# Performance work log

Measured on AMD Instinct MI355X. Metric: run time of the kernel, lower is better.

Reference implementation:

```python
import jax, jax.numpy as jnp
import numpy as np

N = 100_000   # nodes
E = 1_600_000 # message-passing edges
EA = 1_000_000 # aux edges for bilinear head
G = 512       # graphs in batch
F_IN = 16     # num_node_features (fixed in source)
H = 32        # hidden_dim (fixed in source)


def setup_inputs() -> dict:
    key = jax.random.key(0)
    ks = jax.random.split(key, 8)
    x = jax.random.normal(ks[0], (N, F_IN), jnp.float32)
    edge_index = jax.random.randint(ks[1], (2, E), 0, N, dtype=jnp.int32)
    edge_index_aux = jax.random.randint(ks[2], (2, EA), 0, N, dtype=jnp.int32)
    batch = jnp.sort(jax.random.randint(ks[3], (N,), 0, G, dtype=jnp.int32))
    W1 = jax.random.normal(ks[4], (F_IN, H), jnp.float32) / np.sqrt(F_IN)
    b1 = jnp.zeros((H,), jnp.float32)
    W2 = jax.random.normal(ks[5], (H, H), jnp.float32) / np.sqrt(H)
    b2 = jnp.zeros((H,), jnp.float32)
    Wr = jax.random.normal(ks[6], (H, 1), jnp.float32) / np.sqrt(H)
    br = jnp.zeros((1,), jnp.float32)
    Wbil = jax.random.normal(ks[7], (1, H, H), jnp.float32) / H
    bbil = jnp.zeros((1,), jnp.float32)
    return dict(x=x, edge_index=edge_index, edge_index_aux=edge_index_aux,
                batch=batch, W1=W1, b1=b1, W2=W2, b2=b2, Wr=Wr, br=br,
                Wbil=Wbil, bbil=bbil)


def gcn_conv(x, W, b, src, dst):
    # PyG GCNConv: x' = D^{-1/2}(A+I)D^{-1/2} (x W) + b, deg includes self-loop
    xw = x @ W                                                   # [N,H]
    deg = jax.ops.segment_sum(jnp.ones((src.shape[0],), x.dtype), dst,
                              num_segments=N) + 1.0              # +1 self-loop
    dinv = jax.lax.rsqrt(deg)                                    # [N]
    coef = dinv[src] * dinv[dst]                                 # [E]
    agg = jax.ops.segment_sum(xw[src] * coef[:, None], dst, num_segments=N)
    agg = agg + xw * (dinv * dinv)[:, None]                      # self-loop msg
    return agg + b


def reference(x, edge_index, edge_index_aux, batch,
              W1, b1, W2, b2, Wr, br, Wbil, bbil):
    src, dst = edge_index[0], edge_index[1]
    h = jax.nn.relu(gcn_conv(x, W1, b1, src, dst))
    h = gcn_conv(h, W2, b2, src, dst)
    # global_mean_pool over graph ids
    cnt = jax.ops.segment_sum(jnp.ones((N,), h.dtype), batch, num_segments=G)
    pooled = jax.ops.segment_sum(h, batch, num_segments=G) / jnp.maximum(cnt, 1.0)[:, None]
    reg_output = pooled @ Wr + br                                # [G,1]
    # Bilinear edge head: out_e = x1_e^T W x2_e + b
    h1 = h[edge_index_aux[0]]                                    # [EA,H]
    h2 = h[edge_index_aux[1]]                                    # [EA,H]
    edge_pred = jnp.einsum('ei,ij,ej->e', h1, Wbil[0], h2)[:, None] + bbil
    return reg_output, edge_pred
```

## Files before the change

kernel.cpp:

```cpp
#include <hip/hip_runtime.h>
#include <hip/hip_bf16.h>
#include <string.h>
#include <stdint.h>

typedef __hip_bfloat16 bf16;

#define FIN 16
#define H   32
#define PADW 64
#define NB  512
#define BINCAP 4096
#define NPBMAX 200
#define PSTRIDE 65
#define CHUNK 8192
#define SCAN_CHUNK 1024
#define MAXSEG 64
#define POOLBLK 256

__device__ __forceinline__ float b2f(bf16 v) { return __bfloat162float(v); }

__device__ __forceinline__ float loadf(const void* p, size_t i, int f32) {
    return f32 ? ((const float*)p)[i] : b2f(((const bf16*)p)[i]);
}
__device__ __forceinline__ void storef(void* p, size_t i, float v, int f32) {
    if (f32) ((float*)p)[i] = v;
    else     ((bf16*)p)[i] = __float2bfloat16(v);
}

__device__ __forceinline__ unsigned pack2(float lo, float hi) {
    bf16 a = __float2bfloat16(lo), b = __float2bfloat16(hi);
    unsigned short ua, ub;
    memcpy(&ua, &a, 2); memcpy(&ub, &b, 2);
    return ((unsigned)ub << 16) | (unsigned)ua;
}
__device__ __forceinline__ float f_lo(unsigned u) {
    union { unsigned i; float f; } v; v.i = u << 16; return v.f;
}
__device__ __forceinline__ float f_hi(unsigned u) {
    union { unsigned i; float f; } v; v.i = u & 0xffff0000u; return v.f;
}

__global__ void k_detect(const void* __restrict__ x, int nelem, int* __restrict__ flag,
                         float* __restrict__ zf, int nzf,
                         int* __restrict__ zi, int nzi) {
    for (int i = threadIdx.x; i < nzf; i += blockDim.x) zf[i] = 0.f;
    if (zi) for (int i = threadIdx.x; i < nzi; i += blockDim.x) zi[i] = 0;
    __shared__ int cntS;
    if (threadIdx.x == 0) cntS = 0;
    __syncthreads();
    int bad = 0;
    const bf16* p = (const bf16*)x;
    for (int i = threadIdx.x; i < nelem; i += blockDim.x) {
        float v = b2f(p[i]);
        float a = fabsf(v);
        if (isnan(v) || a > 1024.f || (v != 0.f && a < 1e-20f)) bad++;
    }
    atomicAdd(&cntS, bad);
    __syncthreads();
    if (threadIdx.x == 0) flag[0] = (cntS > 64) ? 1 : 0;
}

__global__ void __launch_bounds__(1024) k_p1(
        const int* __restrict__ src, const int* __restrict__ dst,
        int* __restrict__ bincur, unsigned* __restrict__ binbuf,
        int E, int npb) {
    __shared__ int hcnt[4][NB];
    __shared__ int hbase[NB];
    __shared__ int scur[NB];
    int tid = threadIdx.x;
    int grp = tid >> 8;
    int e0 = blockIdx.x * CHUNK;
    int nE = E - e0;
    if (nE > CHUNK) nE = CHUNK;
    for (int i = tid; i < 4 * NB; i += blockDim.x) ((int*)hcnt)[i] = 0;
    __syncthreads();
    for (int i = tid; i < nE; i += blockDim.x)
        atomicAdd(&hcnt[grp][dst[e0 + i] / npb], 1);
    __syncthreads();
    for (int i = tid; i < NB; i += blockDim.x) {
        int c = hcnt[0][i] + hcnt[1][i] + hcnt[2][i] + hcnt[3][i];
        hbase[i] = c ? atomicAdd(&bincur[i], c) : 0;
        scur[i] = 0;
    }
    __syncthreads();
    for (int i = tid; i < nE; i += blockDim.x) {
        int d = dst[e0 + i];
        int bin = d / npb;
        int pos = hbase[bin] + atomicAdd(&scur[bin], 1);
        if (pos < BINCAP)
            binbuf[(size_t)bin * BINCAP + pos] =
                ((unsigned)src[e0 + i] << 10) | (unsigned)(d - bin * npb);
    }
}

__global__ void __launch_bounds__(256) k_p2x(
        const int* __restrict__ bincur, const unsigned* __restrict__ binbuf,
        int* __restrict__ csr, int* __restrict__ deg, float* __restrict__ dinv,
        const void* __restrict__ x, const void* __restrict__ W1,
        const int* __restrict__ flag, unsigned* __restrict__ xsb,
        int N, int npb) {
    __shared__ int cur[NPBMAX];
    __shared__ int psr[NPBMAX * PSTRIDE];
    __shared__ float sW1[FIN * H];
    int f32v = flag[0];
    int b = blockIdx.x;
    int base = b * npb;
    int nn = N - base;
    if (nn > npb) nn = npb;
    if (nn < 0) nn = 0;
    for (int i = threadIdx.x; i < FIN * H; i += blockDim.x) sW1[i] = loadf(W1, i, f32v);
    for (int i = threadIdx.x; i < nn; i += blockDim.x) cur[i] = 0;
    __syncthreads();
    int cnt = bincur[b];
    if (cnt > BINCAP) cnt = BINCAP;
    const unsigned* buf = binbuf + (size_t)b * BINCAP;
    for (int j = threadIdx.x; j < cnt; j += blockDim.x) {
        unsigned p = buf[j];
        int loc = (int)(p & 1023u);
        int s = (int)(p >> 10);
        int pos = atomicAdd(&cur[loc], 1);
        if (pos < PADW) psr[loc * PSTRIDE + pos] = s;
    }
    __syncthreads();
    int tot = nn * PADW;
    for (int idx = threadIdx.x; idx < tot; idx += blockDim.x) {
        int i = idx >> 6, p = idx & 63;
        int dg = cur[i];
        if (dg > PADW) dg = PADW;
        if (p < dg)
            csr[((size_t)(base + i) << 6) + p] = psr[i * PSTRIDE + p];
    }
    for (int i = threadIdx.x; i < nn; i += blockDim.x) {
        int dg = cur[i];
        int n = base + i;
        deg[n] = dg;
        float dv = rsqrtf((float)dg + 1.0f);
        dinv[n] = dv;
        float xr[FIN];
        if (f32v) {
            const float4* xp = (const float4*)((const float*)x + (size_t)n * FIN);
            float4 v0 = xp[0], v1 = xp[1], v2 = xp[2], v3 = xp[3];
            xr[0]=v0.x; xr[1]=v0.y; xr[2]=v0.z; xr[3]=v0.w;
            xr[4]=v1.x; xr[5]=v1.y; xr[6]=v1.z; xr[7]=v1.w;
            xr[8]=v2.x; xr[9]=v2.y; xr[10]=v2.z; xr[11]=v2.w;
            xr[12]=v3.x; xr[13]=v3.y; xr[14]=v3.z; xr[15]=v3.w;
        } else {
            const uint4* xp = (const uint4*)((const bf16*)x + (size_t)n * FIN);
            uint4 u0 = xp[0], u1 = xp[1];
            xr[0]=f_lo(u0.x); xr[1]=f_hi(u0.x); xr[2]=f_lo(u0.y); xr[3]=f_hi(u0.y);
            xr[4]=f_lo(u0.z); xr[5]=f_hi(u0.z); xr[6]=f_lo(u0.w); xr[7]=f_hi(u0.w);
            xr[8]=f_lo(u1.x); xr[9]=f_hi(u1.x); xr[10]=f_lo(u1.y); xr[11]=f_hi(u1.y);
            xr[12]=f_lo(u1.z); xr[13]=f_hi(u1.z); xr[14]=f_lo(u1.w); xr[15]=f_hi(u1.w);
        }
        unsigned outp[16];
#pragma unroll
        for (int jj = 0; jj < 16; jj++) {
            float s0 = 0.f, s1 = 0.f;
#pragma unroll
            for (int f = 0; f < FIN; f++) {
                float xv = xr[f];
                s0 += xv * sW1[f * H + 2 * jj];
                s1 += xv * sW1[f * H + 2 * jj + 1];
            }
            outp[jj] = pack2(s0 * dv, s1 * dv);
        }
        uint4* op = (uint4*)(xsb + (size_t)n * 16);
        op[0] = make_uint4(outp[0], outp[1], outp[2], outp[3]);
        op[1] = make_uint4(outp[4], outp[5], outp[6], outp[7]);
        op[2] = make_uint4(outp[8], outp[9], outp[10], outp[11]);
        op[3] = make_uint4(outp[12], outp[13], outp[14], outp[15]);
    }
}


__global__ void k_fillp(const int* __restrict__ src, const int* __restrict__ dst,
                        int* __restrict__ cursor, int* __restrict__ csr, int E) {
    int e = blockIdx.x * blockDim.x + threadIdx.x;
    if (e >= E) return;
    int d = dst[e];
    int pos = atomicAdd(&cursor[d], 1);
    if (pos < PADW) csr[((size_t)d << 6) + pos] = src[e];
}

__global__ void k_dinvi(const int* __restrict__ deg, float* __restrict__ dinv, int N) {
    int t = blockIdx.x * blockDim.x + threadIdx.x;
    if (t < N) dinv[t] = rsqrtf((float)deg[t] + 1.0f);
}

__global__ void __launch_bounds__(256) k_xw1v(
        const void* __restrict__ x, const void* __restrict__ W1,
        const float* __restrict__ dinv, const int* __restrict__ flag,
        unsigned* __restrict__ xsb, int N) {
    __shared__ float sW[FIN * H];
    __shared__ float sxx[16 * 17];
    int f32 = flag[0];
    for (int i = threadIdx.x; i < FIN * H; i += blockDim.x) sW[i] = loadf(W1, i, f32);
    __syncthreads();
    int t = blockIdx.x * blockDim.x + threadIdx.x;
    int n = t >> 4, j = t & 15, g = threadIdx.x >> 4;
    if (n < N) sxx[g * 17 + j] = loadf(x, (size_t)n * FIN + j, f32);
    __syncthreads();
    if (n >= N) return;
    float dv = dinv[n];
    float s0 = 0.f, s1 = 0.f;
    const float* xp = &sxx[g * 17];
#pragma unroll
    for (int i = 0; i < FIN; i++) {
        float xv = xp[i];
        s0 += xv * sW[i * H + 2 * j];
        s1 += xv * sW[i * H + 2 * j + 1];
    }
    xsb[(size_t)n * 16 + j] = pack2(s0 * dv, s1 * dv);
}

__global__ void __launch_bounds__(256) k_g1(
        const int* __restrict__ deg, const int* __restrict__ csr,
        const float* __restrict__ dinv, const unsigned* __restrict__ xsb,
        const void* __restrict__ W2, const void* __restrict__ b1,
        const int* __restrict__ flag, unsigned* __restrict__ xsb2, int N) {
    __shared__ float sW[H * H];
    __shared__ float sb[H];
    __shared__ float shh[16 * 34];
    int f32 = flag[0];
    for (int i = threadIdx.x; i < H * H; i += blockDim.x) sW[i] = loadf(W2, i, f32);
    if (threadIdx.x < H) sb[threadIdx.x] = loadf(b1, threadIdx.x, f32);
    __syncthreads();
    int t = blockIdx.x * blockDim.x + threadIdx.x;
    int d = t >> 4, j = t & 15, g = threadIdx.x >> 4;
    float dv = 0.f;
    if (d < N) {
        int len = deg[d];
        if (len > PADW) len = PADW;
        const int* lst = csr + ((size_t)d << 6);
        unsigned u = xsb[(size_t)d * 16 + j];
        float a0 = f_lo(u), a1 = f_hi(u);
        float b0 = 0.f, b1v = 0.f;
        int k = 0;
        for (; k + 4 <= len; k += 4) {
            int4 s4 = *(const int4*)(lst + k);
            unsigned u0 = xsb[(size_t)s4.x * 16 + j];
            unsigned u1 = xsb[(size_t)s4.y * 16 + j];
            unsigned u2 = xsb[(size_t)s4.z * 16 + j];
            unsigned u3 = xsb[(size_t)s4.w * 16 + j];
            a0 += f_lo(u0); a1 += f_hi(u0);
            b0 += f_lo(u1); b1v += f_hi(u1);
            a0 += f_lo(u2); a1 += f_hi(u2);
            b0 += f_lo(u3); b1v += f_hi(u3);
        }
        for (; k < len; k++) {
            unsigned u2 = xsb[(size_t)lst[k] * 16 + j];
            a0 += f_lo(u2); a1 += f_hi(u2);
        }
        dv = dinv[d];
        float h0 = (a0 + b0) * dv + sb[2 * j];
        float h1 = (a1 + b1v) * dv + sb[2 * j + 1];
        shh[g * 34 + 2 * j]     = h0 > 0.f ? h0 : 0.f;
        shh[g * 34 + 2 * j + 1] = h1 > 0.f ? h1 : 0.f;
    }
    __syncthreads();
    if (d >= N) return;
    float s0 = 0.f, s1 = 0.f;
    const float* hp = &shh[g * 34];
#pragma unroll
    for (int i = 0; i < H; i++) {
        float hv = hp[i];
        s0 += hv * sW[i * H + 2 * j];
        s1 += hv * sW[i * H + 2 * j + 1];
    }
    xsb2[(size_t)d * 16 + j] = pack2(s0 * dv, s1 * dv);
}

__global__ void __launch_bounds__(256) k_g2(
        const int* __restrict__ deg, const int* __restrict__ csr,
        const float* __restrict__ dinv, const unsigned* __restrict__ xsb2,
        const void* __restrict__ b2v, const void* __restrict__ Wbil,
        const int* __restrict__ batch, const int* __restrict__ flag,
        float* __restrict__ pooled, float* __restrict__ cnt,
        unsigned* __restrict__ hb, unsigned* __restrict__ gb, int N) {
    __shared__ float sW[H * H];
    __shared__ float sb[H];
    __shared__ float shh[16 * 34];
    __shared__ int   sg[16];
    __shared__ float spool[16 * H];
    __shared__ float scnt[16];
    int f32 = flag[0];
    int tid = threadIdx.x;
    for (int i = tid; i < H * H; i += blockDim.x) sW[i] = loadf(Wbil, i, f32);
    if (tid < H) sb[tid] = loadf(b2v, tid, f32);
    for (int i = tid; i < 16 * H; i += blockDim.x) spool[i] = 0.f;
    if (tid < 16) scnt[tid] = 0.f;
    int blk0 = blockIdx.x * 16;
    int nv = N - blk0;
    if (nv > 16) nv = 16;
    if (tid < nv) sg[tid] = batch[blk0 + tid];
    __syncthreads();
    int d = blk0 + (tid >> 4), j = tid & 15, g = tid >> 4;
    float h0 = 0.f, h1 = 0.f;
    int valid = (g < nv);
    if (valid) {
        int len = deg[d];
        if (len > PADW) len = PADW;
        const int* lst = csr + ((size_t)d << 6);
        unsigned u = xsb2[(size_t)d * 16 + j];
        float a0 = f_lo(u), a1 = f_hi(u);
        float b0 = 0.f, b1v = 0.f;
        int k = 0;
        for (; k + 4 <= len; k += 4) {
            int4 s4 = *(const int4*)(lst + k);
            unsigned u0 = xsb2[(size_t)s4.x * 16 + j];
            unsigned u1 = xsb2[(size_t)s4.y * 16 + j];
            unsigned u2 = xsb2[(size_t)s4.z * 16 + j];
            unsigned u3 = xsb2[(size_t)s4.w * 16 + j];
            a0 += f_lo(u0); a1 += f_hi(u0);
            b0 += f_lo(u1); b1v += f_hi(u1);
            a0 += f_lo(u2); a1 += f_hi(u2);
            b0 += f_lo(u3); b1v += f_hi(u3);
        }
        for (; k < len; k++) {
            unsigned u2 = xsb2[(size_t)lst[k] * 16 + j];
            a0 += f_lo(u2); a1 += f_hi(u2);
        }
        float dv = dinv[d];
        h0 = (a0 + b0) * dv + sb[2 * j];
        h1 = (a1 + b1v) * dv + sb[2 * j + 1];
        hb[(size_t)d * 16 + j] = pack2(h0, h1);
        shh[g * 34 + 2 * j]     = h0;
        shh[g * 34 + 2 * j + 1] = h1;
    }
    int g0 = sg[0];
    int nseg = sg[nv - 1] - g0 + 1;
    if (valid) {
        int sgn = sg[g];
        if (nseg <= 16) {
            atomicAdd(&spool[(sgn - g0) * H + 2 * j], h0);
            atomicAdd(&spool[(sgn - g0) * H + 2 * j + 1], h1);
            if (j == 0) atomicAdd(&scnt[sgn - g0], 1.f);
        } else {
            atomicAdd(&pooled[(size_t)sgn * H + 2 * j], h0);
            atomicAdd(&pooled[(size_t)sgn * H + 2 * j + 1], h1);
            if (j == 0) atomicAdd(&cnt[sgn], 1.f);
        }
    }
    __syncthreads();
    if (nseg <= 16) {
        for (int i = tid; i < nseg * H; i += blockDim.x) {
            float v = spool[i];
            if (v != 0.f) atomicAdd(&pooled[(size_t)(g0 + (i >> 5)) * H + (i & 31)], v);
        }
        for (int i = tid; i < nseg; i += blockDim.x)
            if (scnt[i] != 0.f) atomicAdd(&cnt[g0 + i], scnt[i]);
    }
    if (!valid) return;
    float s0 = 0.f, s1 = 0.f;
    const float* hp = &shh[g * 34];
#pragma unroll
    for (int i = 0; i < H; i++) {
        float hv = hp[i];
        s0 += hv * sW[i * H + 2 * j];
        s1 += hv * sW[i * H + 2 * j + 1];
    }
    gb[(size_t)d * 16 + j] = pack2(s0, s1);
}

__global__ void __launch_bounds__(512) k_poolhb(
        const void* __restrict__ b2v, const void* __restrict__ Wbil,
        const int* __restrict__ batch, const int* __restrict__ flag,
        const float* __restrict__ aggB, float* __restrict__ pooled,
        float* __restrict__ cnt, bf16* __restrict__ hb, bf16* __restrict__ gb,
        int N) {
    __shared__ float sW[H * H];
    __shared__ float sb[H];
    __shared__ float sh[POOLBLK][H];
    __shared__ int   sg[POOLBLK];
    __shared__ float spool[MAXSEG * H];
    __shared__ float scnt[MAXSEG];
    int f32 = flag[0];
    int tid = threadIdx.x;
    for (int i = tid; i < H * H; i += blockDim.x) sW[i] = loadf(Wbil, i, f32);
    if (tid < H) sb[tid] = loadf(b2v, tid, f32);
    int blk0 = blockIdx.x * POOLBLK;
    int nvalid = N - blk0;
    if (nvalid > POOLBLK) nvalid = POOLBLK;
    if (tid < nvalid) sg[tid] = batch[blk0 + tid];
    for (int i = tid; i < MAXSEG * H; i += blockDim.x) spool[i] = 0.f;
    if (tid < MAXSEG) scnt[tid] = 0.f;
    __syncthreads();
    int f = tid & 31, k = tid >> 5;
    for (int r = k; r < nvalid; r += 16) {
        float v = aggB[(size_t)(blk0 + r) * H + f] + sb[f];
        sh[r][f] = v;
        hb[(size_t)(blk0 + r) * H + f] = __float2bfloat16(v);
    }
    __syncthreads();
    int g0 = sg[0];
    int nseg = sg[nvalid - 1] - g0 + 1;
    if (nseg <= MAXSEG) {
        for (int r = k; r < nvalid; r += 16) {
            int gl = sg[r] - g0;
            atomicAdd(&spool[gl * H + f], sh[r][f]);
            if (f == 0) atomicAdd(&scnt[gl], 1.f);
        }
    } else {
        for (int r = k; r < nvalid; r += 16) {
            atomicAdd(&pooled[(size_t)sg[r] * H + f], sh[r][f]);
            if (f == 0) atomicAdd(&cnt[sg[r]], 1.f);
        }
    }
    for (int r = k; r < nvalid; r += 16) {
        float s = 0.f;
#pragma unroll
        for (int i = 0; i < H; i++) s += sh[r][i] * sW[i * H + f];
        gb[(size_t)(blk0 + r) * H + f] = __float2bfloat16(s);
    }
    if (nseg <= MAXSEG) {
        __syncthreads();
        for (int i = tid; i < nseg * H; i += blockDim.x)
            atomicAdd(&pooled[(size_t)(g0 + (i >> 5)) * H + (i & 31)], spool[i]);
        for (int i = tid; i < nseg; i += blockDim.x)
            atomicAdd(&cnt[g0 + i], scnt[i]);
    }
}


__global__ void k_degi(const int* __restrict__ dst, int* __restrict__ deg, int E) {
    int t = blockIdx.x * blockDim.x + threadIdx.x;
    if (t < E) atomicAdd(&deg[dst[t]], 1);
}

__global__ void k_scan1(const int* __restrict__ deg, int* __restrict__ partials, int N) {
    __shared__ int sd[256];
    int base = blockIdx.x * SCAN_CHUNK + threadIdx.x * 4;
    int s = 0;
#pragma unroll
    for (int k = 0; k < 4; k++) { int i = base + k; s += (i < N) ? deg[i] : 0; }
    sd[threadIdx.x] = s;
    __syncthreads();
    for (int off = 128; off > 0; off >>= 1) {
        if (threadIdx.x < off) sd[threadIdx.x] += sd[threadIdx.x + off];
        __syncthreads();
    }
    if (threadIdx.x == 0) partials[blockIdx.x] = sd[0];
}

__global__ void k_scan2(const int* __restrict__ partials, int* __restrict__ chunk_off, int B1) {
    __shared__ int sd[256];
    int t = threadIdx.x;
    int lv[4];
    int s = 0;
#pragma unroll
    for (int k = 0; k < 4; k++) { int i = t * 4 + k; lv[k] = (i < B1) ? partials[i] : 0; s += lv[k]; }
    sd[t] = s;
    __syncthreads();
    int inc = s;
    for (int off = 1; off < 256; off <<= 1) {
        int v = (t >= off) ? sd[t - off] : 0;
        __syncthreads();
        sd[t] += v;
        __syncthreads();
    }
    int run = sd[t] - inc;
#pragma unroll
    for (int k = 0; k < 4; k++) { int i = t * 4 + k; if (i < B1) chunk_off[i] = run; run += lv[k]; }
    if (t == 255) chunk_off[B1] = run;
}

__global__ void k_scan3(const int* __restrict__ deg, const int* __restrict__ chunk_off,
                        int* __restrict__ row_ptr, int* __restrict__ cursor,
                        int N, int E) {
    __shared__ int sd[256];
    int t = threadIdx.x;
    int base = blockIdx.x * SCAN_CHUNK + t * 4;
    int lv[4];
    int s = 0;
#pragma unroll
    for (int k = 0; k < 4; k++) { int i = base + k; lv[k] = (i < N) ? deg[i] : 0; s += lv[k]; }
    sd[t] = s;
    __syncthreads();
    int inc = s;
    for (int off = 1; off < 256; off <<= 1) {
        int v = (t >= off) ? sd[t - off] : 0;
        __syncthreads();
        sd[t] += v;
        __syncthreads();
    }
    int run = chunk_off[blockIdx.x] + sd[t] - inc;
#pragma unroll
    for (int k = 0; k < 4; k++) {
        int i = base + k;
        if (i < N) { row_ptr[i] = run; cursor[i] = run; }
        run += lv[k];
    }
    if (blockIdx.x == 0 && t == 0) row_ptr[N] = E;
}

__global__ void k_fill(const int* __restrict__ src, const int* __restrict__ dst,
                       int* __restrict__ cursor, int* __restrict__ csr, int E) {
    int e = blockIdx.x * blockDim.x + threadIdx.x;
    if (e >= E) return;
    int pos = atomicAdd(&cursor[dst[e]], 1);
    csr[pos] = src[e];
}

__global__ void k_gather(const int* __restrict__ row_ptr, const int* __restrict__ csr,
                         const float* __restrict__ dinv, const float* __restrict__ xs,
                         float* __restrict__ agg, int N) {
    int t = blockIdx.x * blockDim.x + threadIdx.x;
    int d = t >> 5, f = t & 31;
    if (d >= N) return;
    int beg = row_ptr[d], end = row_ptr[d + 1];
    float acc  = xs[(size_t)d * H + f];
    float acc2 = 0.f;
    int j = beg;
    for (; j + 1 < end; j += 2) {
        int s0 = csr[j], s1 = csr[j + 1];
        acc  += xs[(size_t)s0 * H + f];
        acc2 += xs[(size_t)s1 * H + f];
    }
    if (j < end) acc += xs[(size_t)csr[j] * H + f];
    agg[(size_t)d * H + f] = (acc + acc2) * dinv[d];
}

__global__ void k_xw1n(const void* __restrict__ x, const void* __restrict__ W1,
                       const float* __restrict__ dinv, const int* __restrict__ flag,
                       float* __restrict__ xs, int N) {
    __shared__ float sW[FIN * H];
    int f32 = flag[0];
    for (int i = threadIdx.x; i < FIN * H; i += blockDim.x) sW[i] = loadf(W1, i, f32);
    __syncthreads();
    int n = blockIdx.x * blockDim.x + threadIdx.x;
    if (n >= N) return;
    float xr[FIN];
#pragma unroll
    for (int i = 0; i < FIN; i++) xr[i] = loadf(x, (size_t)n * FIN + i, f32);
    float dv = dinv[n];
#pragma unroll
    for (int f = 0; f < H; f++) {
        float s = 0.f;
#pragma unroll
        for (int i = 0; i < FIN; i++) s += xr[i] * sW[i * H + f];
        xs[(size_t)n * H + f] = s * dv;
    }
}

__global__ void k_h1xw2n(const void* __restrict__ W2, const void* __restrict__ b1,
                         const float* __restrict__ dinv, const int* __restrict__ flag,
                         const float* __restrict__ agg, float* __restrict__ xs2, int N) {
    __shared__ float sW[H * H];
    __shared__ float sb[H];
    int f32 = flag[0];
    for (int i = threadIdx.x; i < H * H; i += blockDim.x) sW[i] = loadf(W2, i, f32);
    if (threadIdx.x < H) sb[threadIdx.x] = loadf(b1, threadIdx.x, f32);
    __syncthreads();
    int n = blockIdx.x * blockDim.x + threadIdx.x;
    if (n >= N) return;
    float hr[H];
#pragma unroll
    for (int f = 0; f < H; f++) {
        float v = agg[(size_t)n * H + f] + sb[f];
        hr[f] = v > 0.f ? v : 0.f;
    }
    float dv = dinv[n];
#pragma unroll
    for (int f = 0; f < H; f++) {
        float s = 0.f;
#pragma unroll
        for (int i = 0; i < H; i++) s += hr[i] * sW[i * H + f];
        xs2[(size_t)n * H + f] = s * dv;
    }
}


__global__ void k_degf(const int* __restrict__ dst, float* __restrict__ deg, int E) {
    int t = blockIdx.x * blockDim.x + threadIdx.x;
    if (t < E) atomicAdd(&deg[dst[t]], 1.0f);
}
__global__ void k_dinvf(float* __restrict__ deg, int N) {
    int t = blockIdx.x * blockDim.x + threadIdx.x;
    if (t < N) deg[t] = rsqrtf(deg[t] + 1.0f);
}
__global__ void k_xw1o(const void* __restrict__ x, const void* __restrict__ W1,
                       const float* __restrict__ dinv, const int* __restrict__ flag,
                       float* __restrict__ xw, float* __restrict__ agg, int N) {
    __shared__ float sW[FIN * H];
    int f32 = flag[0];
    for (int i = threadIdx.x; i < FIN * H; i += blockDim.x) sW[i] = loadf(W1, i, f32);
    __syncthreads();
    int n = blockIdx.x * blockDim.x + threadIdx.x;
    if (n >= N) return;
    float xr[FIN];
#pragma unroll
    for (int i = 0; i < FIN; i++) xr[i] = loadf(x, (size_t)n * FIN + i, f32);
    float dv = dinv[n], dv2 = dv * dv;
#pragma unroll
    for (int f = 0; f < H; f++) {
        float s = 0.f;
#pragma unroll
        for (int i = 0; i < FIN; i++) s += xr[i] * sW[i * H + f];
        xw[(size_t)n * H + f]  = s;
        agg[(size_t)n * H + f] = s * dv2;
    }
}
__global__ void k_scatter(const int* __restrict__ src, const int* __restrict__ dst,
                          const float* __restrict__ dinv, const float* __restrict__ xw,
                          float* __restrict__ agg, int E) {
    int t = blockIdx.x * blockDim.x + threadIdx.x;
    int e = t >> 5, f = t & 31;
    if (e >= E) return;
    int s = src[e], d = dst[e];
    float c = dinv[s] * dinv[d];
    atomicAdd(&agg[(size_t)d * H + f], xw[(size_t)s * H + f] * c);
}
__global__ void k_h1xw2o(const void* __restrict__ W2, const void* __restrict__ b1,
                         const float* __restrict__ dinv, const int* __restrict__ flag,
                         float* __restrict__ aggio, float* __restrict__ xw2, int N) {
    __shared__ float sW[H * H];
    __shared__ float sb[H];
    int f32 = flag[0];
    for (int i = threadIdx.x; i < H * H; i += blockDim.x) sW[i] = loadf(W2, i, f32);
    if (threadIdx.x < H) sb[threadIdx.x] = loadf(b1, threadIdx.x, f32);
    __syncthreads();
    int n = blockIdx.x * blockDim.x + threadIdx.x;
    if (n >= N) return;
    float hr[H];
#pragma unroll
    for (int f = 0; f < H; f++) {
        float v = aggio[(size_t)n * H + f] + sb[f];
        hr[f] = v > 0.f ? v : 0.f;
    }
    float dv = dinv[n], dv2 = dv * dv;
#pragma unroll
    for (int f = 0; f < H; f++) {
        float s = 0.f;
#pragma unroll
        for (int i = 0; i < H; i++) s += hr[i] * sW[i * H + f];
        xw2[(size_t)n * H + f]   = s;
        aggio[(size_t)n * H + f] = s * dv2;
    }
}


__global__ void k_bilreg(const int* __restrict__ srcA, const int* __restrict__ dstA,
                         const unsigned* __restrict__ gb32, const unsigned* __restrict__ hb32,
                         const void* __restrict__ bbil,
                         const float* __restrict__ pooled, const float* __restrict__ cnt,
                         const void* __restrict__ Wr, const void* __restrict__ br,
                         const int* __restrict__ flag, void* __restrict__ out,
                         int G, int EA) {
    int f32 = flag[0];
    int t = blockIdx.x * blockDim.x + threadIdx.x;
    if (t < EA) {
        int s = srcA[t], d = dstA[t];
        const uint4* gp = (const uint4*)(gb32 + (size_t)s * (H / 2));
        const uint4* hp = (const uint4*)(hb32 + (size_t)d * (H / 2));
        float acc = 0.f;
#pragma unroll
        for (int kk = 0; kk < 4; kk++) {
            uint4 a = gp[kk], b = hp[kk];
            acc += f_lo(a.x) * f_lo(b.x) + f_hi(a.x) * f_hi(b.x);
            acc += f_lo(a.y) * f_lo(b.y) + f_hi(a.y) * f_hi(b.y);
            acc += f_lo(a.z) * f_lo(b.z) + f_hi(a.z) * f_hi(b.z);
            acc += f_lo(a.w) * f_lo(b.w) + f_hi(a.w) * f_hi(b.w);
        }
        storef(out, (size_t)G + t, acc + loadf(bbil, 0, f32), f32);
    } else {
        int g = t - EA;
        if (g < G) {
            float c = cnt[g];
            c = c > 1.f ? c : 1.f;
            float s = 0.f;
#pragma unroll
            for (int i = 0; i < H; i++) s += pooled[(size_t)g * H + i] * loadf(Wr, i, f32);
            storef(out, g, s / c + loadf(br, 0, f32), f32);
        }
    }
}

extern "C" void kernel_launch(void* const* d_in, const int* in_sizes, int n_in,
                              void* d_out, int out_size, void* d_ws, size_t ws_size,
                              hipStream_t stream) {
    const void* x     = d_in[0];
    const int*  ei    = (const int*)d_in[1];
    const int*  eia   = (const int*)d_in[2];
    const int*  batch = (const int*)d_in[3];
    const void* W1    = d_in[4];
    const void* b1    = d_in[5];
    const void* W2    = d_in[6];
    const void* b2    = d_in[7];
    const void* Wr    = d_in[8];
    const void* br    = d_in[9];
    const void* Wbil  = d_in[10];
    const void* bbil  = d_in[11];

    const int N  = in_sizes[0] / FIN;
    const int E  = in_sizes[1] / 2;
    const int EA = in_sizes[2] / 2;
    const int G  = out_size - EA;

    float* ws     = (float*)d_ws;
    int*   flag   = (int*)ws;
    float* dinv   = ws + 16;
    float* A      = dinv + N;
    float* B      = A + (size_t)N * H;
    float* pooled = B + (size_t)N * H;
    float* cnt    = pooled + (size_t)G * H;
    float* fend   = cnt + G;

    unsigned* xsb  = (unsigned*)B;
    unsigned* xsb2 = (unsigned*)B + (size_t)N * 16;
    unsigned* hb32 = (unsigned*)A;
    unsigned* gb32 = hb32 + (size_t)N * (H / 2);

    int* degA   = (int*)fend;
    int* csrA   = (int*)(((uintptr_t)(degA + N) + 15) & ~(uintptr_t)15);
    int* bincur = csrA + (size_t)N * PADW;
    size_t needA  = (size_t)((char*)bincur - (char*)d_ws);
    size_t needA2 = (size_t)((char*)(bincur + NB) - (char*)d_ws);
    const int B1 = (N + SCAN_CHUNK - 1) / SCAN_CHUNK;
    int* deg_i     = (int*)fend;
    int* curB      = deg_i + N;
    int* row_ptr   = curB + N;
    int* chunk_off = row_ptr + N + 1;
    int* csrB      = chunk_off + B1 + 1;
    size_t needB = (size_t)((char*)(csrB + E) - (char*)d_ws);

    const int npb = (N + NB - 1) / NB;
    const bool tierA2 = (ws_size >= needA2) && (npb <= NPBMAX) && (N <= (1 << 22)) &&
                        ((size_t)NB * BINCAP <= (size_t)N * H * 2);
    const bool tierA  = !tierA2 && (ws_size >= needA);
    const bool tierB  = !tierA2 && !tierA && (ws_size >= needB) && (B1 <= 1024);

    const int* src  = ei;
    const int* dst  = ei + E;
    const int* srcA = eia;
    const int* dstA = eia + EA;

    const int TB = 256;
    const int npool = G * H + G;

    k_detect<<<1, 1024, 0, stream>>>(x, 1024, flag, pooled, npool,
                                     (tierA2 || tierA) ? bincur : (int*)nullptr,
                                     tierA2 ? NB : 0);

    int ggrid16 = (int)(((long)N * 16 + TB - 1) / TB);
    int ggrid32 = (int)(((long)N * 32 + TB - 1) / TB);
    int ngrid   = (N + TB - 1) / TB;

    if (tierA2) {
        unsigned* binbuf = (unsigned*)A;
        int nblk1 = (E + CHUNK - 1) / CHUNK;
        k_p1<<<nblk1, 1024, 0, stream>>>(src, dst, bincur, binbuf, E, npb);
        k_p2x<<<NB, TB, 0, stream>>>(bincur, binbuf, csrA, degA, dinv,
                                     x, W1, flag, xsb, N, npb);
        k_g1<<<ggrid16, TB, 0, stream>>>(degA, csrA, dinv, xsb, W2, b1, flag, xsb2, N);
        k_g2<<<ggrid16, TB, 0, stream>>>(degA, csrA, dinv, xsb2, b2, Wbil, batch, flag,
                                         pooled, cnt, hb32, gb32, N);
    } else if (tierA) {
        hipMemsetAsync(degA, 0, (size_t)N * sizeof(int), stream);
        k_fillp<<<(E + TB - 1) / TB, TB, 0, stream>>>(src, dst, degA, csrA, E);
        k_dinvi<<<ngrid, TB, 0, stream>>>(degA, dinv, N);
        k_xw1v<<<ggrid16, TB, 0, stream>>>(x, W1, dinv, flag, xsb, N);
        k_g1<<<ggrid16, TB, 0, stream>>>(degA, csrA, dinv, xsb, W2, b1, flag, xsb2, N);
        k_g2<<<ggrid16, TB, 0, stream>>>(degA, csrA, dinv, xsb2, b2, Wbil, batch, flag,
                                         pooled, cnt, hb32, gb32, N);
    } else if (tierB) {
        hipMemsetAsync(deg_i, 0, (size_t)N * sizeof(int), stream);
        k_degi<<<(E + TB - 1) / TB, TB, 0, stream>>>(dst, deg_i, E);
        k_dinvi<<<ngrid, TB, 0, stream>>>(deg_i, dinv, N);
        k_scan1<<<B1, TB, 0, stream>>>(deg_i, chunk_off, N);
        k_scan2<<<1, TB, 0, stream>>>(chunk_off, chunk_off, B1);
        k_scan3<<<B1, TB, 0, stream>>>(deg_i, chunk_off, row_ptr, curB, N, E);
        k_fill<<<(E + TB - 1) / TB, TB, 0, stream>>>(src, dst, curB, csrB, E);
        k_xw1n<<<ngrid, TB, 0, stream>>>(x, W1, dinv, flag, A, N);
        k_gather<<<ggrid32, TB, 0, stream>>>(row_ptr, csrB, dinv, A, B, N);
        k_h1xw2n<<<ngrid, TB, 0, stream>>>(W2, b1, dinv, flag, B, A, N);
        k_gather<<<ggrid32, TB, 0, stream>>>(row_ptr, csrB, dinv, A, B, N);
        k_poolhb<<<(N + POOLBLK - 1) / POOLBLK, 512, 0, stream>>>(
            b2, Wbil, batch, flag, B, pooled, cnt, (bf16*)hb32, (bf16*)gb32, N);
    } else {
        hipMemsetAsync(dinv, 0, (size_t)N * sizeof(float), stream);
        k_degf<<<(E + TB - 1) / TB, TB, 0, stream>>>(dst, dinv, E);
        k_dinvf<<<ngrid, TB, 0, stream>>>(dinv, N);
        k_xw1o<<<ngrid, TB, 0, stream>>>(x, W1, dinv, flag, A, B, N);
        long tot = (long)E * 32;
        int sgrid = (int)((tot + TB - 1) / TB);
        k_scatter<<<sgrid, TB, 0, stream>>>(src, dst, dinv, A, B, E);
        k_h1xw2o<<<ngrid, TB, 0, stream>>>(W2, b1, dinv, flag, B, A, N);
        k_scatter<<<sgrid, TB, 0, stream>>>(src, dst, dinv, A, B, E);
        k_poolhb<<<(N + POOLBLK - 1) / POOLBLK, 512, 0, stream>>>(
            b2, Wbil, batch, flag, B, pooled, cnt, (bf16*)hb32, (bf16*)gb32, N);
    }

    k_bilreg<<<(EA + G + TB - 1) / TB, TB, 0, stream>>>(
        srcA, dstA, gb32, hb32, bbil, pooled, cnt, Wr, br, flag, d_out, G, EA);
}
```

Measured before the change: 265.1 us.

## Phase source-range gathers for cache locality in GCN aggregation kernels

Replaces the per-node gather kernels with persistent-style kernels in which each 16-lane group handles eight consecutive destination nodes. Each group sweeps the neighbor lists four times, each time reading only sources inside one quarter of the node range, so concurrently resident waves touch a smaller slice of the feature table and it stays in cache. The dense 32x32 matvec now uses lane shuffles instead of shared memory, and pooling accumulates runs of equal graph ids in registers before issuing atomics. In exchange, the CSR index lists are read four times per node, every edge pays a range-check branch, and the grid is capped, which may reduce parallelism.

```diff
diff --git a/kernel.cpp b/kernel.cpp
--- a/kernel.cpp
+++ b/kernel.cpp
@@ -16,6 +16,11 @@
 #define SCAN_CHUNK 1024
 #define MAXSEG 64
 #define POOLBLK 256
+#define NPT 8
+#define GPHASES 4
+#define GMAXBLK 1024
+
+typedef int vi4 __attribute__((ext_vector_type(4)));
 
 __device__ __forceinline__ float b2f(bf16 v) { return __bfloat162float(v); }
 
@@ -213,64 +218,93 @@
     xsb[(size_t)n * 16 + j] = pack2(s0 * dv, s1 * dv);
 }
 
-__global__ void __launch_bounds__(256) k_g1(
+#define GATHER_PHASE(TBL, i)                                                  \
+    {                                                                         \
+        int d_ = base + (i);                                                  \
+        if (d_ < N) {                                                         \
+            const int* lst = csr + ((size_t)d_ << 6);                         \
+            int len = lenr[i];                                                \
+            int k = 0;                                                        \
+            for (; k + 4 <= len; k += 4) {                                    \
+                vi4 s4 = *(const vi4*)(lst + k);                              \
+                if ((unsigned)(s4.x - lo) < span) {                           \
+                    unsigned u = TBL[(size_t)s4.x * 16 + j];                  \
+                    a0[i] += f_lo(u); a1[i] += f_hi(u); }                     \
+                if ((unsigned)(s4.y - lo) < span) {                           \
+                    unsigned u = TBL[(size_t)s4.y * 16 + j];                  \
+                    a0[i] += f_lo(u); a1[i] += f_hi(u); }                     \
+                if ((unsigned)(s4.z - lo) < span) {                           \
+                    unsigned u = TBL[(size_t)s4.z * 16 + j];                  \
+                    a0[i] += f_lo(u); a1[i] += f_hi(u); }                     \
+                if ((unsigned)(s4.w - lo) < span) {                           \
+                    unsigned u = TBL[(size_t)s4.w * 16 + j];                  \
+                    a0[i] += f_lo(u); a1[i] += f_hi(u); }                     \
+            }                                                                 \
+            for (; k < len; k++) {                                            \
+                int s_ = lst[k];                                              \
+                if ((unsigned)(s_ - lo) < span) {                             \
+                    unsigned u = TBL[(size_t)s_ * 16 + j];                    \
+                    a0[i] += f_lo(u); a1[i] += f_hi(u); }                     \
+            }                                                                 \
+        }                                                                     \
+    }
+
+__global__ void __launch_bounds__(256, 4) k_g1c(
         const int* __restrict__ deg, const int* __restrict__ csr,
         const float* __restrict__ dinv, const unsigned* __restrict__ xsb,
         const void* __restrict__ W2, const void* __restrict__ b1,
         const int* __restrict__ flag, unsigned* __restrict__ xsb2, int N) {
     __shared__ float sW[H * H];
     __shared__ float sb[H];
-    __shared__ float shh[16 * 34];
     int f32 = flag[0];
     for (int i = threadIdx.x; i < H * H; i += blockDim.x) sW[i] = loadf(W2, i, f32);
     if (threadIdx.x < H) sb[threadIdx.x] = loadf(b1, threadIdx.x, f32);
     __syncthreads();
-    int t = blockIdx.x * blockDim.x + threadIdx.x;
-    int d = t >> 4, j = t & 15, g = threadIdx.x >> 4;
-    float dv = 0.f;
-    if (d < N) {
-        int len = deg[d];
-        if (len > PADW) len = PADW;
-        const int* lst = csr + ((size_t)d << 6);
-        unsigned u = xsb[(size_t)d * 16 + j];
-        float a0 = f_lo(u), a1 = f_hi(u);
-        float b0 = 0.f, b1v = 0.f;
-        int k = 0;
-        for (; k + 4 <= len; k += 4) {
-            int4 s4 = *(const int4*)(lst + k);
-            unsigned u0 = xsb[(size_t)s4.x * 16 + j];
-            unsigned u1 = xsb[(size_t)s4.y * 16 + j];
-            unsigned u2 = xsb[(size_t)s4.z * 16 + j];
-            unsigned u3 = xsb[(size_t)s4.w * 16 + j];
-            a0 += f_lo(u0); a1 += f_hi(u0);
-            b0 += f_lo(u1); b1v += f_hi(u1);
-            a0 += f_lo(u2); a1 += f_hi(u2);
-            b0 += f_lo(u3); b1v += f_hi(u3);
-        }
-        for (; k < len; k++) {
-            unsigned u2 = xsb[(size_t)lst[k] * 16 + j];
-            a0 += f_lo(u2); a1 += f_hi(u2);
-        }
-        dv = dinv[d];
-        float h0 = (a0 + b0) * dv + sb[2 * j];
-        float h1 = (a1 + b1v) * dv + sb[2 * j + 1];
-        shh[g * 34 + 2 * j]     = h0 > 0.f ? h0 : 0.f;
-        shh[g * 34 + 2 * j + 1] = h1 > 0.f ? h1 : 0.f;
-    }
-    __syncthreads();
-    if (d >= N) return;
-    float s0 = 0.f, s1 = 0.f;
-    const float* hp = &shh[g * 34];
-#pragma unroll
-    for (int i = 0; i < H; i++) {
-        float hv = hp[i];
-        s0 += hv * sW[i * H + 2 * j];
-        s1 += hv * sW[i * H + 2 * j + 1];
-    }
-    xsb2[(size_t)d * 16 + j] = pack2(s0 * dv, s1 * dv);
-}
-
-__global__ void __launch_bounds__(256) k_g2(
+    int j = threadIdx.x & 15;
+    int grp = threadIdx.x >> 4;
+    for (int base = (blockIdx.x * 16 + grp) * NPT; base < N;
+         base += gridDim.x * 16 * NPT) {
+        float a0[NPT], a1[NPT];
+        int lenr[NPT];
+#pragma unroll
+        for (int i = 0; i < NPT; i++) {
+            a0[i] = 0.f; a1[i] = 0.f; lenr[i] = 0;
+            int d = base + i;
+            if (d < N) {
+                int l = deg[d];
+                lenr[i] = l > PADW ? PADW : l;
+                unsigned u = xsb[(size_t)d * 16 + j];
+                a0[i] = f_lo(u); a1[i] = f_hi(u);
+            }
+        }
+        for (int ph = 0; ph < GPHASES; ph++) {
+            int lo = (int)(((long)N * ph) / GPHASES);
+            int hi = (int)(((long)N * (ph + 1)) / GPHASES);
+            unsigned span = (unsigned)(hi - lo);
+#pragma unroll
+            for (int i = 0; i < NPT; i++) GATHER_PHASE(xsb, i)
+        }
+#pragma unroll
+        for (int i = 0; i < NPT; i++) {
+            int d = base + i;
+            if (d >= N) continue;
+            float dv = dinv[d];
+            float h0 = a0[i] * dv + sb[2 * j];  h0 = h0 > 0.f ? h0 : 0.f;
+            float h1 = a1[i] * dv + sb[2 * j + 1]; h1 = h1 > 0.f ? h1 : 0.f;
+            float s0 = 0.f, s1 = 0.f;
+#pragma unroll
+            for (int l = 0; l < 16; l++) {
+                float hv0 = __shfl(h0, l, 16);
+                float hv1 = __shfl(h1, l, 16);
+                s0 += hv0 * sW[(2 * l) * H + 2 * j] + hv1 * sW[(2 * l + 1) * H + 2 * j];
+                s1 += hv0 * sW[(2 * l) * H + 2 * j + 1] + hv1 * sW[(2 * l + 1) * H + 2 * j + 1];
+            }
+            xsb2[(size_t)d * 16 + j] = pack2(s0 * dv, s1 * dv);
+        }
+    }
+}
+
+__global__ void __launch_bounds__(256, 4) k_g2c(
         const int* __restrict__ deg, const int* __restrict__ csr,
         const float* __restrict__ dinv, const unsigned* __restrict__ xsb2,
         const void* __restrict__ b2v, const void* __restrict__ Wbil,
@@ -279,87 +313,69 @@
         unsigned* __restrict__ hb, unsigned* __restrict__ gb, int N) {
     __shared__ float sW[H * H];
     __shared__ float sb[H];
-    __shared__ float shh[16 * 34];
-    __shared__ int   sg[16];
-    __shared__ float spool[16 * H];
-    __shared__ float scnt[16];
     int f32 = flag[0];
-    int tid = threadIdx.x;
-    for (int i = tid; i < H * H; i += blockDim.x) sW[i] = loadf(Wbil, i, f32);
-    if (tid < H) sb[tid] = loadf(b2v, tid, f32);
-    for (int i = tid; i < 16 * H; i += blockDim.x) spool[i] = 0.f;
-    if (tid < 16) scnt[tid] = 0.f;
-    int blk0 = blockIdx.x * 16;
-    int nv = N - blk0;
-    if (nv > 16) nv = 16;
-    if (tid < nv) sg[tid] = batch[blk0 + tid];
-    __syncthreads();
-    int d = blk0 + (tid >> 4), j = tid & 15, g = tid >> 4;
-    float h0 = 0.f, h1 = 0.f;
-    int valid = (g < nv);
-    if (valid) {
-        int len = deg[d];
-        if (len > PADW) len = PADW;
-        const int* lst = csr + ((size_t)d << 6);
-        unsigned u = xsb2[(size_t)d * 16 + j];
-        float a0 = f_lo(u), a1 = f_hi(u);
-        float b0 = 0.f, b1v = 0.f;
-        int k = 0;
-        for (; k + 4 <= len; k += 4) {
-            int4 s4 = *(const int4*)(lst + k);
-            unsigned u0 = xsb2[(size_t)s4.x * 16 + j];
-            unsigned u1 = xsb2[(size_t)s4.y * 16 + j];
-            unsigned u2 = xsb2[(size_t)s4.z * 16 + j];
-            unsigned u3 = xsb2[(size_t)s4.w * 16 + j];
-            a0 += f_lo(u0); a1 += f_hi(u0);
-            b0 += f_lo(u1); b1v += f_hi(u1);
-            a0 += f_lo(u2); a1 += f_hi(u2);
-            b0 += f_lo(u3); b1v += f_hi(u3);
-        }
-        for (; k < len; k++) {
-            unsigned u2 = xsb2[(size_t)lst[k] * 16 + j];
-            a0 += f_lo(u2); a1 += f_hi(u2);
-        }
-        float dv = dinv[d];
-        h0 = (a0 + b0) * dv + sb[2 * j];
-        h1 = (a1 + b1v) * dv + sb[2 * j + 1];
-        hb[(size_t)d * 16 + j] = pack2(h0, h1);
-        shh[g * 34 + 2 * j]     = h0;
-        shh[g * 34 + 2 * j + 1] = h1;
-    }
-    int g0 = sg[0];
-    int nseg = sg[nv - 1] - g0 + 1;
-    if (valid) {
-        int sgn = sg[g];
-        if (nseg <= 16) {
-            atomicAdd(&spool[(sgn - g0) * H + 2 * j], h0);
-            atomicAdd(&spool[(sgn - g0) * H + 2 * j + 1], h1);
-            if (j == 0) atomicAdd(&scnt[sgn - g0], 1.f);
-        } else {
-            atomicAdd(&pooled[(size_t)sgn * H + 2 * j], h0);
-            atomicAdd(&pooled[(size_t)sgn * H + 2 * j + 1], h1);
-            if (j == 0) atomicAdd(&cnt[sgn], 1.f);
-        }
-    }
-    __syncthreads();
-    if (nseg <= 16) {
-        for (int i = tid; i < nseg * H; i += blockDim.x) {
-            float v = spool[i];
-            if (v != 0.f) atomicAdd(&pooled[(size_t)(g0 + (i >> 5)) * H + (i & 31)], v);
-        }
-        for (int i = tid; i < nseg; i += blockDim.x)
-            if (scnt[i] != 0.f) atomicAdd(&cnt[g0 + i], scnt[i]);
-    }
-    if (!valid) return;
-    float s0 = 0.f, s1 = 0.f;
-    const float* hp = &shh[g * 34];
-#pragma unroll
-    for (int i = 0; i < H; i++) {
-        float hv = hp[i];
-        s0 += hv * sW[i * H + 2 * j];
-        s1 += hv * sW[i * H + 2 * j + 1];
-    }
-    gb[(size_t)d * 16 + j] = pack2(s0, s1);
+    for (int i = threadIdx.x; i < H * H; i += blockDim.x) sW[i] = loadf(Wbil, i, f32);
+    if (threadIdx.x < H) sb[threadIdx.x] = loadf(b2v, threadIdx.x, f32);
+    __syncthreads();
+    int j = threadIdx.x & 15;
+    int grp = threadIdx.x >> 4;
+    for (int base = (blockIdx.x * 16 + grp) * NPT; base < N;
+         base += gridDim.x * 16 * NPT) {
+        float a0[NPT], a1[NPT];
+        int lenr[NPT];
+#pragma unroll
+        for (int i = 0; i < NPT; i++) {
+            a0[i] = 0.f; a1[i] = 0.f; lenr[i] = 0;
+            int d = base + i;
+            if (d < N) {
+                int l = deg[d];
+                lenr[i] = l > PADW ? PADW : l;
+                unsigned u = xsb2[(size_t)d * 16 + j];
+                a0[i] = f_lo(u); a1[i] = f_hi(u);
+            }
+        }
+        for (int ph = 0; ph < GPHASES; ph++) {
+            int lo = (int)(((long)N * ph) / GPHASES);
+            int hi = (int)(((long)N * (ph + 1)) / GPHASES);
+            unsigned span = (unsigned)(hi - lo);
+#pragma unroll
+            for (int i = 0; i < NPT; i++) GATHER_PHASE(xsb2, i)
+        }
+        int curg = -1;
+        float p0 = 0.f, p1 = 0.f, runc = 0.f;
+#pragma unroll
+        for (int i = 0; i < NPT; i++) {
+            int d = base + i;
+            if (d >= N) continue;
+            float dv = dinv[d];
+            float h0 = a0[i] * dv + sb[2 * j];
+            float h1 = a1[i] * dv + sb[2 * j + 1];
+            hb[(size_t)d * 16 + j] = pack2(h0, h1);
+            int bg = batch[d];
+            if (bg != curg) {
+                if (curg >= 0) {
+                    atomicAdd(&pooled[(size_t)curg * H + 2 * j], p0);
+                    atomicAdd(&pooled[(size_t)curg * H + 2 * j + 1], p1);
+                    if (j == 0) atomicAdd(&cnt[curg], runc);
+                }
+                curg = bg; p0 = h0; p1 = h1; runc = 1.f;
+            } else { p0 += h0; p1 += h1; runc += 1.f; }
+            float s0 = 0.f, s1 = 0.f;
+#pragma unroll
+            for (int l = 0; l < 16; l++) {
+                float hv0 = __shfl(h0, l, 16);
+                float hv1 = __shfl(h1, l, 16);
+                s0 += hv0 * sW[(2 * l) * H + 2 * j] + hv1 * sW[(2 * l + 1) * H + 2 * j];
+                s1 += hv0 * sW[(2 * l) * H + 2 * j + 1] + hv1 * sW[(2 * l + 1) * H + 2 * j + 1];
+            }
+            gb[(size_t)d * 16 + j] = pack2(s0, s1);
+        }
+        if (curg >= 0) {
+            atomicAdd(&pooled[(size_t)curg * H + 2 * j], p0);
+            atomicAdd(&pooled[(size_t)curg * H + 2 * j + 1], p1);
+            if (j == 0) atomicAdd(&cnt[curg], runc);
+        }
+    }
 }
 
 __global__ void __launch_bounds__(512) k_poolhb(
@@ -745,23 +761,27 @@
     int ggrid32 = (int)(((long)N * 32 + TB - 1) / TB);
     int ngrid   = (N + TB - 1) / TB;
 
+    int nblkG = (N + 16 * NPT - 1) / (16 * NPT);
+    if (nblkG > GMAXBLK) nblkG = GMAXBLK;
+    if (nblkG < 1) nblkG = 1;
+
     if (tierA2) {
         unsigned* binbuf = (unsigned*)A;
         int nblk1 = (E + CHUNK - 1) / CHUNK;
         k_p1<<<nblk1, 1024, 0, stream>>>(src, dst, bincur, binbuf, E, npb);
         k_p2x<<<NB, TB, 0, stream>>>(bincur, binbuf, csrA, degA, dinv,
                                      x, W1, flag, xsb, N, npb);
-        k_g1<<<ggrid16, TB, 0, stream>>>(degA, csrA, dinv, xsb, W2, b1, flag, xsb2, N);
-        k_g2<<<ggrid16, TB, 0, stream>>>(degA, csrA, dinv, xsb2, b2, Wbil, batch, flag,
-                                         pooled, cnt, hb32, gb32, N);
+        k_g1c<<<nblkG, TB, 0, stream>>>(degA, csrA, dinv, xsb, W2, b1, flag, xsb2, N);
+        k_g2c<<<nblkG, TB, 0, stream>>>(degA, csrA, dinv, xsb2, b2, Wbil, batch, flag,
+                                        pooled, cnt, hb32, gb32, N);
     } else if (tierA) {
         hipMemsetAsync(degA, 0, (size_t)N * sizeof(int), stream);
         k_fillp<<<(E + TB - 1) / TB, TB, 0, stream>>>(src, dst, degA, csrA, E);
         k_dinvi<<<ngrid, TB, 0, stream>>>(degA, dinv, N);
         k_xw1v<<<ggrid16, TB, 0, stream>>>(x, W1, dinv, flag, xsb, N);
-        k_g1<<<ggrid16, TB, 0, stream>>>(degA, csrA, dinv, xsb, W2, b1, flag, xsb2, N);
-        k_g2<<<ggrid16, TB, 0, stream>>>(degA, csrA, dinv, xsb2, b2, Wbil, batch, flag,
-                                         pooled, cnt, hb32, gb32, N);
+        k_g1c<<<nblkG, TB, 0, stream>>>(degA, csrA, dinv, xsb, W2, b1, flag, xsb2, N);
+        k_g2c<<<nblkG, TB, 0, stream>>>(degA, csrA, dinv, xsb2, b2, Wbil, batch, flag,
+                                        pooled, cnt, hb32, gb32, N);
     } else if (tierB) {
         hipMemsetAsync(deg_i, 0, (size_t)N * sizeof(int), stream);
         k_degi<<<(E + TB - 1) / TB, TB, 0, stream>>>(dst, deg_i, E);
```

New measurement: 591.0 us. 123% more time.
